# Kernel optimization log

Hardware: AMD Instinct MI355X
Metric: run time of the kernel (lower is better)

Reference implementation:

```python
import jax, jax.numpy as jnp
import numpy as np

N = 10000          # num_stations / nodes
E = 320000         # edges
IN_DIM = 32
HID = 64
SEQ = 168
OUT_DIM = 10000


def _gcn_conv(x, W, b, src, dst, num_nodes):
    """PyG GCNConv: add self-loops, sym-normalize, gather-scatter aggregate."""
    loop = jnp.arange(num_nodes)
    s = jnp.concatenate([src, loop])
    d = jnp.concatenate([dst, loop])
    deg = jax.ops.segment_sum(jnp.ones_like(d, dtype=x.dtype), d, num_segments=num_nodes)
    dinv = jnp.where(deg > 0, jax.lax.rsqrt(deg), 0.0)
    norm = dinv[s] * dinv[d]                      # [E+N]
    h = x @ W.T                                   # [N, out] linear (no bias inside)
    msg = h[s] * norm[:, None]                    # gather + scale
    out = jax.ops.segment_sum(msg, d, num_segments=num_nodes)  # scatter-add
    return out + b


def setup_inputs() -> dict:
    key = jax.random.key(0)
    ks = jax.random.split(key, 16)
    sc = 0.05
    return {
        "x": jax.random.normal(ks[0], (N, IN_DIM), jnp.float32),
        "edge_index": jax.random.randint(ks[1], (2, E), 0, N, jnp.int64),
        "rain_history": jax.random.normal(ks[2], (1, SEQ), jnp.float32),
        "future_rain": jax.random.normal(ks[3], (1, 1), jnp.float32),
        "W1": jax.random.normal(ks[4], (HID, IN_DIM), jnp.float32) * sc,
        "b1": jnp.zeros((HID,), jnp.float32),
        "W2": jax.random.normal(ks[5], (HID, HID), jnp.float32) * sc,
        "b2": jnp.zeros((HID,), jnp.float32),
        "wf1_W": jax.random.normal(ks[6], (HID, SEQ + 1), jnp.float32) * sc,
        "wf1_b": jnp.zeros((HID,), jnp.float32),
        "wf2_W": jax.random.normal(ks[7], (HID, HID), jnp.float32) * sc,
        "wf2_b": jnp.zeros((HID,), jnp.float32),
        "of1_W": jax.random.normal(ks[8], (HID * 2, HID * N + HID), jnp.float32) * 0.001,
        "of1_b": jnp.zeros((HID * 2,), jnp.float32),
        "of2_W": jax.random.normal(ks[9], (OUT_DIM, HID * 2), jnp.float32) * sc,
        "of2_b": jnp.zeros((OUT_DIM,), jnp.float32),
    }


def reference(x, edge_index, rain_history, future_rain,
              W1, b1, W2, b2, wf1_W, wf1_b, wf2_W, wf2_b,
              of1_W, of1_b, of2_W, of2_b):
    src, dst = edge_index[0], edge_index[1]
    num_nodes = x.shape[0]
    h = jax.nn.relu(_gcn_conv(x, W1, b1, src, dst, num_nodes))
    h = jax.nn.relu(_gcn_conv(h, W2, b2, src, dst, num_nodes))
    h = jnp.clip(h, -10.0, 10.0)
    node_features = h.reshape(1, -1)                        # [1, N*HID]
    weather_input = jnp.concatenate([rain_history, future_rain], axis=1)  # [1, SEQ+1]
    w = jax.nn.relu(weather_input @ wf1_W.T + wf1_b)
    weather_features = w @ wf2_W.T + wf2_b                  # [1, HID]
    combined = jnp.concatenate([node_features, weather_features], axis=1)
    o = jax.nn.relu(combined @ of1_W.T + of1_b)
    out = o @ of2_W.T + of2_b                               # [1, OUT_DIM]
    return out.squeeze(0)
```

## Files before the change

kernel.cpp:

```cpp
#include <hip/hip_runtime.h>

#define N_NODES 10000
#define N_EDGES 320000
#define HID 64
#define IN_DIM 32
#define SEQ 168
#define OUT_DIM 10000
#define OF1_COLS 640064
#define NODE_COLS 640000
#define NODE_NV   160000
#define OF1_SPLITS 64
#define OF1_CHUNK  2500
#define OF1_ROWS   8
#define BUCKET 128
#define FILLB  1250
#define LIN1B  2500

typedef __attribute__((ext_vector_type(4))) float f32x4;

__global__ __launch_bounds__(256) void k_fill_lin1_weather(
        const int* __restrict__ eidx, int* __restrict__ cursor, int* __restrict__ csr,
        const float* __restrict__ x, const float* __restrict__ W1, float* __restrict__ hlin,
        const float* __restrict__ rain, const float* __restrict__ fut,
        const float* __restrict__ w1W, const float* __restrict__ w1b,
        const float* __restrict__ w2W, const float* __restrict__ w2b,
        const float* __restrict__ of1W, float* __restrict__ wtail) {
    int t = threadIdx.x;
    int b = blockIdx.x;
    if (b < FILLB) {
        int e = b * 256 + t;
        if (e < N_EDGES) {
            int s = eidx[e];
            int d = eidx[N_EDGES + e];
            int slot = atomicAdd(&cursor[d], 1);
            csr[d * BUCKET + slot] = s;
        }
    } else if (b < FILLB + LIN1B) {
        __shared__ float Wl[64][33];
        __shared__ float xs[4][32];
        for (int i = t; i < 64 * 32; i += 256) Wl[i >> 5][i & 31] = W1[i];
        int node0 = (b - FILLB) * 4;
        if (t < 128) {
            int n = t >> 5, k = t & 31;
            xs[n][k] = x[(node0 + n) * IN_DIM + k];
        }
        __syncthreads();
        int nl = t >> 6, j = t & 63;
        float acc = 0.f;
#pragma unroll
        for (int k = 0; k < 32; k++) acc += xs[nl][k] * Wl[j][k];
        hlin[(node0 + nl) * HID + j] = acc;
    } else {
        __shared__ float wi[SEQ + 1];
        __shared__ float w1[64];
        __shared__ float wf[64];
        if (t < SEQ) wi[t] = rain[t];
        if (t == SEQ) wi[SEQ] = fut[0];
        __syncthreads();
        if (t < 64) {
            float acc = w1b[t];
            for (int i = 0; i < SEQ + 1; i++) acc += w1W[t * (SEQ + 1) + i] * wi[i];
            w1[t] = fmaxf(acc, 0.f);
        }
        __syncthreads();
        if (t < 64) {
            float acc2 = w2b[t];
#pragma unroll
            for (int i = 0; i < 64; i++) acc2 += w2W[t * 64 + i] * w1[i];
            wf[t] = acc2;
        }
        __syncthreads();
        if (t < 128) {
            const float* Wt = of1W + (size_t)t * OF1_COLS + NODE_COLS;
            float s = 0.f;
#pragma unroll
            for (int w = 0; w < 64; w++) s += Wt[w] * wf[w];
            wtail[t] = s;
        }
    }
}

__global__ __launch_bounds__(256) void k_agg1_lin2(
        const float* __restrict__ hlin, const int* __restrict__ cnt,
        const int* __restrict__ csr, const float* __restrict__ b1,
        const float* __restrict__ W2, float* __restrict__ h2) {
    __shared__ float Wl[64][65];
    __shared__ float xs[4][64];
    int t = threadIdx.x;
    for (int i = t; i < 64 * 64; i += 256) Wl[i >> 6][i & 63] = W2[i];
    int wid = t >> 6, lane = t & 63;
    int n = blockIdx.x * 4 + wid;
    int deg = cnt[n];
    float dn = rsqrtf((float)(deg + 1));
    float acc = hlin[n * HID + lane] * dn;
    const int* row = csr + n * BUCKET;
    for (int base = 0; base < deg; base += 64) {
        int idx = base + lane;
        int sv = row[(idx < deg) ? idx : 0];
        float dv = (idx < deg) ? rsqrtf((float)(cnt[sv] + 1)) : 0.f;
        int m = deg - base;
        if (m > 64) m = 64;
        int m4 = (m + 3) & ~3;
        for (int j = 0; j < m4; j += 4) {
            int s0 = __shfl(sv, j, 64), s1 = __shfl(sv, j + 1, 64);
            int s2 = __shfl(sv, j + 2, 64), s3 = __shfl(sv, j + 3, 64);
            float d0 = __shfl(dv, j, 64), d1 = __shfl(dv, j + 1, 64);
            float d2 = __shfl(dv, j + 2, 64), d3 = __shfl(dv, j + 3, 64);
            float v0 = hlin[s0 * HID + lane];
            float v1 = hlin[s1 * HID + lane];
            float v2 = hlin[s2 * HID + lane];
            float v3 = hlin[s3 * HID + lane];
            acc = fmaf(d0, v0, acc);
            acc = fmaf(d1, v1, acc);
            acc = fmaf(d2, v2, acc);
            acc = fmaf(d3, v3, acc);
        }
    }
    float v = fmaxf(dn * acc + b1[lane], 0.f);
    xs[wid][lane] = v;
    __syncthreads();
    float a2 = 0.f;
#pragma unroll
    for (int k = 0; k < 64; k++) a2 += xs[wid][k] * Wl[lane][k];
    h2[n * HID + lane] = a2;
}

__global__ __launch_bounds__(256) void k_agg2(
        const float* __restrict__ h2, const int* __restrict__ cnt,
        const int* __restrict__ csr, const float* __restrict__ b2,
        float* __restrict__ comb) {
    int t = threadIdx.x;
    int wid = t >> 6, lane = t & 63;
    int n = blockIdx.x * 4 + wid;
    int deg = cnt[n];
    float dn = rsqrtf((float)(deg + 1));
    float acc = h2[n * HID + lane] * dn;
    const int* row = csr + n * BUCKET;
    for (int base = 0; base < deg; base += 64) {
        int idx = base + lane;
        int sv = row[(idx < deg) ? idx : 0];
        float dv = (idx < deg) ? rsqrtf((float)(cnt[sv] + 1)) : 0.f;
        int m = deg - base;
        if (m > 64) m = 64;
        int m4 = (m + 3) & ~3;
        for (int j = 0; j < m4; j += 4) {
            int s0 = __shfl(sv, j, 64), s1 = __shfl(sv, j + 1, 64);
            int s2 = __shfl(sv, j + 2, 64), s3 = __shfl(sv, j + 3, 64);
            float d0 = __shfl(dv, j, 64), d1 = __shfl(dv, j + 1, 64);
            float d2 = __shfl(dv, j + 2, 64), d3 = __shfl(dv, j + 3, 64);
            float v0 = h2[s0 * HID + lane];
            float v1 = h2[s1 * HID + lane];
            float v2 = h2[s2 * HID + lane];
            float v3 = h2[s3 * HID + lane];
            acc = fmaf(d0, v0, acc);
            acc = fmaf(d1, v1, acc);
            acc = fmaf(d2, v2, acc);
            acc = fmaf(d3, v3, acc);
        }
    }
    float v = dn * acc + b2[lane];
    v = fmaxf(v, 0.f);
    v = fminf(v, 10.f);
    comb[n * HID + lane] = v;
}

__global__ __launch_bounds__(256) void k_of1(const float* __restrict__ W, const float* __restrict__ comb,
                                             float* __restrict__ o_pre) {
    int split = blockIdx.x;
    int j0 = blockIdx.y * OF1_ROWS;
    int i0 = split * OF1_CHUNK;
    int i1 = i0 + OF1_CHUNK;
    const f32x4* C4 = (const f32x4*)comb;
    const f32x4* Wr[OF1_ROWS];
#pragma unroll
    for (int r = 0; r < OF1_ROWS; r++)
        Wr[r] = (const f32x4*)(W + (size_t)(j0 + r) * OF1_COLS);
    float a[OF1_ROWS];
#pragma unroll
    for (int r = 0; r < OF1_ROWS; r++) a[r] = 0.f;
    for (int i = i0 + threadIdx.x; i < i1; i += 256) {
        f32x4 cv = C4[i];
#pragma unroll
        for (int r = 0; r < OF1_ROWS; r++) {
            f32x4 wv = __builtin_nontemporal_load(&Wr[r][i]);
            a[r] += wv.x * cv.x + wv.y * cv.y + wv.z * cv.z + wv.w * cv.w;
        }
    }
#pragma unroll
    for (int off = 1; off < 64; off <<= 1) {
#pragma unroll
        for (int r = 0; r < OF1_ROWS; r++) a[r] += __shfl_xor(a[r], off, 64);
    }
    __shared__ float red[4][OF1_ROWS];
    int lane = threadIdx.x & 63, wid = threadIdx.x >> 6;
    if (lane == 0) {
#pragma unroll
        for (int r = 0; r < OF1_ROWS; r++) red[wid][r] = a[r];
    }
    __syncthreads();
    if (threadIdx.x < OF1_ROWS)
        atomicAdd(&o_pre[j0 + threadIdx.x],
                  red[0][threadIdx.x] + red[1][threadIdx.x] + red[2][threadIdx.x] + red[3][threadIdx.x]);
}

__global__ __launch_bounds__(256) void k_of2(const float* __restrict__ W, const float* __restrict__ of2b,
                                             const float* __restrict__ o_pre, const float* __restrict__ of1b,
                                             const float* __restrict__ wtail, float* __restrict__ out) {
    __shared__ float os[128];
    int t = threadIdx.x;
    if (t < 128) os[t] = fmaxf(o_pre[t] + of1b[t] + wtail[t], 0.f);
    __syncthreads();
    int k = blockIdx.x * 256 + t;
    if (k >= OUT_DIM) return;
    const f32x4* Wr = (const f32x4*)(W + (size_t)k * 128);
    float acc = of2b[k];
#pragma unroll
    for (int i = 0; i < 32; i++) {
        f32x4 wv = __builtin_nontemporal_load(&Wr[i]);
        int base = i * 4;
        acc += wv.x * os[base + 0] + wv.y * os[base + 1] + wv.z * os[base + 2] + wv.w * os[base + 3];
    }
    out[k] = acc;
}

extern "C" void kernel_launch(void* const* d_in, const int* in_sizes, int n_in,
                              void* d_out, int out_size, void* d_ws, size_t ws_size,
                              hipStream_t stream) {
    const float* x    = (const float*)d_in[0];
    const int*  eidx  = (const int*)d_in[1];
    const float* rain = (const float*)d_in[2];
    const float* fut  = (const float*)d_in[3];
    const float* W1   = (const float*)d_in[4];
    const float* b1   = (const float*)d_in[5];
    const float* W2   = (const float*)d_in[6];
    const float* b2   = (const float*)d_in[7];
    const float* wf1W = (const float*)d_in[8];
    const float* wf1b = (const float*)d_in[9];
    const float* wf2W = (const float*)d_in[10];
    const float* wf2b = (const float*)d_in[11];
    const float* of1W = (const float*)d_in[12];
    const float* of1b = (const float*)d_in[13];
    const float* of2W = (const float*)d_in[14];
    const float* of2b = (const float*)d_in[15];
    float* out = (float*)d_out;

    char* p = (char*)d_ws;
    int*   cursor = (int*)(p + 0);
    float* o_pre  = (float*)(p + 40000);
    int*   csr    = (int*)(p + 40960);
    float* hlin   = (float*)(p + 5242880);
    float* h2     = (float*)(p + 7864320);
    float* comb   = (float*)(p + 10485760);
    float* wtail  = (float*)(p + 13107200);

    hipMemsetAsync(p, 0, 40512, stream);

    k_fill_lin1_weather<<<FILLB + LIN1B + 1, 256, 0, stream>>>(
        eidx, cursor, csr, x, W1, hlin, rain, fut, wf1W, wf1b, wf2W, wf2b, of1W, wtail);

    k_agg1_lin2<<<N_NODES / 4, 256, 0, stream>>>(hlin, cursor, csr, b1, W2, h2);
    k_agg2<<<N_NODES / 4, 256, 0, stream>>>(h2, cursor, csr, b2, comb);

    k_of1<<<dim3(OF1_SPLITS, 128 / OF1_ROWS), 256, 0, stream>>>(of1W, comb, o_pre);
    k_of2<<<(OUT_DIM + 255) / 256, 256, 0, stream>>>(of2W, of2b, o_pre, of1b, wtail, out);
}
```

Before: 520.9 us.

## Fuse second GCN aggregation with of1 matvec using slotted atomic partial sums

The second aggregation kernel now feeds its 4 node feature vectors (256 columns) from shared memory directly into the of1 matvec. Each block reads the matching 256-column slice of all 128 of1 rows and reduces it with wave shuffles. Partial sums are atomically added into one of 64 slot buffers, and k_of2 sums those slots. This removes the comb buffer round trip and one kernel launch, and lets the large of1 weight stream overlap with aggregation work. In exchange, there are far more atomics (2500 blocks × 128 rows), and each block reads only short 1KB row segments, which may coalesce less well.

```diff
diff --git a/kernel.cpp b/kernel.cpp
--- a/kernel.cpp
+++ b/kernel.cpp
@@ -8,13 +8,10 @@
 #define OUT_DIM 10000
 #define OF1_COLS 640064
 #define NODE_COLS 640000
-#define NODE_NV   160000
-#define OF1_SPLITS 64
-#define OF1_CHUNK  2500
-#define OF1_ROWS   8
 #define BUCKET 128
 #define FILLB  1250
 #define LIN1B  2500
+#define NSLOT  64
 
 typedef __attribute__((ext_vector_type(4))) float f32x4;
 
@@ -125,10 +122,11 @@
     h2[n * HID + lane] = a2;
 }
 
-__global__ __launch_bounds__(256) void k_agg2(
+__global__ __launch_bounds__(256) void k_agg2_of1(
         const float* __restrict__ h2, const int* __restrict__ cnt,
         const int* __restrict__ csr, const float* __restrict__ b2,
-        float* __restrict__ comb) {
+        const float* __restrict__ of1W, float* __restrict__ o_pre) {
+    __shared__ float xs[4][64];
     int t = threadIdx.x;
     int wid = t >> 6, lane = t & 63;
     int n = blockIdx.x * 4 + wid;
@@ -161,46 +159,46 @@
     float v = dn * acc + b2[lane];
     v = fmaxf(v, 0.f);
     v = fminf(v, 10.f);
-    comb[n * HID + lane] = v;
-}
-
-__global__ __launch_bounds__(256) void k_of1(const float* __restrict__ W, const float* __restrict__ comb,
-                                             float* __restrict__ o_pre) {
-    int split = blockIdx.x;
-    int j0 = blockIdx.y * OF1_ROWS;
-    int i0 = split * OF1_CHUNK;
-    int i1 = i0 + OF1_CHUNK;
-    const f32x4* C4 = (const f32x4*)comb;
-    const f32x4* Wr[OF1_ROWS];
-#pragma unroll
-    for (int r = 0; r < OF1_ROWS; r++)
-        Wr[r] = (const f32x4*)(W + (size_t)(j0 + r) * OF1_COLS);
-    float a[OF1_ROWS];
-#pragma unroll
-    for (int r = 0; r < OF1_ROWS; r++) a[r] = 0.f;
-    for (int i = i0 + threadIdx.x; i < i1; i += 256) {
-        f32x4 cv = C4[i];
-#pragma unroll
-        for (int r = 0; r < OF1_ROWS; r++) {
-            f32x4 wv = __builtin_nontemporal_load(&Wr[r][i]);
-            a[r] += wv.x * cv.x + wv.y * cv.y + wv.z * cv.z + wv.w * cv.w;
-        }
-    }
-#pragma unroll
-    for (int off = 1; off < 64; off <<= 1) {
-#pragma unroll
-        for (int r = 0; r < OF1_ROWS; r++) a[r] += __shfl_xor(a[r], off, 64);
-    }
-    __shared__ float red[4][OF1_ROWS];
-    int lane = threadIdx.x & 63, wid = threadIdx.x >> 6;
-    if (lane == 0) {
-#pragma unroll
-        for (int r = 0; r < OF1_ROWS; r++) red[wid][r] = a[r];
-    }
+    xs[wid][lane] = v;
     __syncthreads();
-    if (threadIdx.x < OF1_ROWS)
-        atomicAdd(&o_pre[j0 + threadIdx.x],
-                  red[0][threadIdx.x] + red[1][threadIdx.x] + red[2][threadIdx.x] + red[3][threadIdx.x]);
+
+    f32x4 c = ((const f32x4*)xs)[lane];
+    size_t colbase = (size_t)blockIdx.x * 256;
+    float* oslot = o_pre + (size_t)(blockIdx.x & (NSLOT - 1)) * 128;
+    int j0w = wid * 32;
+#pragma unroll 2
+    for (int g = 0; g < 8; g++) {
+        int j0 = j0w + g * 4;
+        const f32x4* W0 = (const f32x4*)(of1W + (size_t)(j0 + 0) * OF1_COLS + colbase);
+        const f32x4* W1r = (const f32x4*)(of1W + (size_t)(j0 + 1) * OF1_COLS + colbase);
+        const f32x4* W2r = (const f32x4*)(of1W + (size_t)(j0 + 2) * OF1_COLS + colbase);
+        const f32x4* W3r = (const f32x4*)(of1W + (size_t)(j0 + 3) * OF1_COLS + colbase);
+        f32x4 w0 = __builtin_nontemporal_load(&W0[lane]);
+        f32x4 w1 = __builtin_nontemporal_load(&W1r[lane]);
+        f32x4 w2 = __builtin_nontemporal_load(&W2r[lane]);
+        f32x4 w3 = __builtin_nontemporal_load(&W3r[lane]);
+        float a0 = w0.x * c.x + w0.y * c.y + w0.z * c.z + w0.w * c.w;
+        float a1 = w1.x * c.x + w1.y * c.y + w1.z * c.z + w1.w * c.w;
+        float a2 = w2.x * c.x + w2.y * c.y + w2.z * c.z + w2.w * c.w;
+        float a3 = w3.x * c.x + w3.y * c.y + w3.z * c.z + w3.w * c.w;
+        float a0s = a0 + __shfl_xor(a0, 32, 64);
+        float a1s = a1 + __shfl_xor(a1, 32, 64);
+        float a2s = a2 + __shfl_xor(a2, 32, 64);
+        float a3s = a3 + __shfl_xor(a3, 32, 64);
+        float c01 = (lane < 32) ? a0s : a1s;
+        float c23 = (lane < 32) ? a2s : a3s;
+        float c01b = c01 + __shfl_xor(c01, 16, 64);
+        float c23b = c23 + __shfl_xor(c23, 16, 64);
+        float e = ((lane & 16) == 0) ? c01b : c23b;
+        e += __shfl_xor(e, 8, 64);
+        e += __shfl_xor(e, 4, 64);
+        e += __shfl_xor(e, 2, 64);
+        e += __shfl_xor(e, 1, 64);
+        if ((lane & 15) == 0) {
+            int roff = ((lane & 16) ? 2 : 0) + ((lane & 32) ? 1 : 0);
+            atomicAdd(&oslot[j0 + roff], e);
+        }
+    }
 }
 
 __global__ __launch_bounds__(256) void k_of2(const float* __restrict__ W, const float* __restrict__ of2b,
@@ -208,7 +206,12 @@
                                              const float* __restrict__ wtail, float* __restrict__ out) {
     __shared__ float os[128];
     int t = threadIdx.x;
-    if (t < 128) os[t] = fmaxf(o_pre[t] + of1b[t] + wtail[t], 0.f);
+    if (t < 128) {
+        float s = of1b[t] + wtail[t];
+#pragma unroll
+        for (int cidx = 0; cidx < NSLOT; cidx++) s += o_pre[cidx * 128 + t];
+        os[t] = fmaxf(s, 0.f);
+    }
     __syncthreads();
     int k = blockIdx.x * 256 + t;
     if (k >= OUT_DIM) return;
@@ -247,20 +250,18 @@
     char* p = (char*)d_ws;
     int*   cursor = (int*)(p + 0);
     float* o_pre  = (float*)(p + 40000);
-    int*   csr    = (int*)(p + 40960);
+    int*   csr    = (int*)(p + 73728);
     float* hlin   = (float*)(p + 5242880);
     float* h2     = (float*)(p + 7864320);
-    float* comb   = (float*)(p + 10485760);
-    float* wtail  = (float*)(p + 13107200);
-
-    hipMemsetAsync(p, 0, 40512, stream);
+    float* wtail  = (float*)(p + 10485760);
+
+    hipMemsetAsync(p, 0, 72768, stream);
 
     k_fill_lin1_weather<<<FILLB + LIN1B + 1, 256, 0, stream>>>(
         eidx, cursor, csr, x, W1, hlin, rain, fut, wf1W, wf1b, wf2W, wf2b, of1W, wtail);
 
     k_agg1_lin2<<<N_NODES / 4, 256, 0, stream>>>(hlin, cursor, csr, b1, W2, h2);
-    k_agg2<<<N_NODES / 4, 256, 0, stream>>>(h2, cursor, csr, b2, comb);
-
-    k_of1<<<dim3(OF1_SPLITS, 128 / OF1_ROWS), 256, 0, stream>>>(of1W, comb, o_pre);
+    k_agg2_of1<<<N_NODES / 4, 256, 0, stream>>>(h2, cursor, csr, b2, of1W, o_pre);
+
     k_of2<<<(OUT_DIM + 255) / 256, 256, 0, stream>>>(of2W, of2b, o_pre, of1b, wtail, out);
 }
```

New measurement: 510.5 us. -2.0%, faster.
